# Kernel tuning notes

Hardware: AMD Instinct MI355X
Metric: run time of the kernel (lower is better)

Reference implementation:

```python
import jax, jax.numpy as jnp
import numpy as np

NUM_HEADS = 8
BLOCK_SIZE = 32   # tokens per block
WINDOW = 64       # window radius in blocks -> attends to blocks [i-64, i+64]


def setup_inputs() -> dict:
    key = jax.random.key(0)
    ks = jax.random.split(key, 5)
    B, N, C = 8, 8192, 512
    s = 0.02
    return {
        "x": jax.random.normal(ks[0], (B, N, C), dtype=jnp.float32),
        # torch Linear(dim, 3*dim): y = x @ W.T + b; we store W already transposed [in, out]
        "W_qkv": jax.random.normal(ks[1], (C, 3 * C), dtype=jnp.float32) * s,
        "b_qkv": jax.random.normal(ks[2], (3 * C,), dtype=jnp.float32) * s,
        "W_proj": jax.random.normal(ks[3], (C, C), dtype=jnp.float32) * s,
        "b_proj": jax.random.normal(ks[4], (C,), dtype=jnp.float32) * s,
    }


def reference(x, W_qkv, b_qkv, W_proj, b_proj):
    B, N, C = x.shape
    h = NUM_HEADS
    dh = C // h
    scale = jnp.asarray(dh, x.dtype) ** -0.5

    # qkv projection, then the module's head-interleaved split:
    # rearrange 'b n (h d) -> b h n d' with d = 3C/h, chunk(3) on last dim,
    # rearrange back 'b h n d -> b n (h d)'. Equivalent to:
    qkv = (x @ W_qkv + b_qkv).reshape(B, N, h, 3 * dh)
    q = qkv[..., :dh].reshape(B, N, C)
    k = qkv[..., dh:2 * dh].reshape(B, N, C)
    v = qkv[..., 2 * dh:].reshape(B, N, C)

    # dynamic blocking (N chosen divisible by BLOCK_SIZE -> no padding)
    nb = N // BLOCK_SIZE
    qb = q.reshape(B, nb, BLOCK_SIZE, C)
    kb = k.reshape(B, nb, BLOCK_SIZE, C)
    vb = v.reshape(B, nb, BLOCK_SIZE, C)

    # per-offset block attention: query block i, position s attends to
    # position s of every block j in [i-WINDOW, i+WINDOW]
    attn = jnp.einsum('bisc,bjsc->bisj', qb, kb) * scale  # [B, nb, s, nb]
    i_idx = jnp.arange(nb)[:, None]
    j_idx = jnp.arange(nb)[None, :]
    band = (j_idx >= i_idx - WINDOW) & (j_idx <= i_idx + WINDOW)  # [nb, nb]
    neg = jnp.finfo(attn.dtype).min
    attn = jnp.where(band[None, :, None, :], attn, neg)
    attn = jax.nn.softmax(attn, axis=-1)
    out = jnp.einsum('bisj,bjsc->bisc', attn, vb)  # [B, nb, s, C]
    out = out.reshape(B, N, C)

    # 'b n (h d) -> b n h d -> b n (h d)' is the identity
    return out @ W_proj + b_proj
```

## Files before the change

### kernel.cpp

```cpp
#include <hip/hip_runtime.h>
#include <hip/hip_bf16.h>
#include <stdint.h>

#define B_   8
#define N_   8192
#define C_   512
#define NB   256
#define WIN  64

typedef __attribute__((ext_vector_type(8))) short short8;
typedef __attribute__((ext_vector_type(4))) float f32x4;
typedef __hip_bfloat16 bf16;

__device__ __forceinline__ void gload_lds16(const void* g, void* l) {
  __builtin_amdgcn_global_load_lds((const __attribute__((address_space(1))) void*)g,
                                   (__attribute__((address_space(3))) void*)l, 16, 0, 0);
}

__device__ __forceinline__ f32x4 mfma16(short8 a, short8 b, f32x4 c) {
  return __builtin_amdgcn_mfma_f32_16x16x32_bf16(a, b, c, 0, 0, 0);
}


__global__ __launch_bounds__(256) void k_conv_x(const float4* __restrict__ x,
                                                ushort4* __restrict__ xb) {
  size_t idx = (size_t)blockIdx.x * 256 + threadIdx.x;
  float4 v = x[idx];
  union { ushort4 u; bf16 b[4]; } o;
  o.b[0] = __float2bfloat16(v.x); o.b[1] = __float2bfloat16(v.y);
  o.b[2] = __float2bfloat16(v.z); o.b[3] = __float2bfloat16(v.w);
  xb[idx] = o.u;
}

__global__ __launch_bounds__(256) void k_conv_w(const float* __restrict__ W,
                                                const float* __restrict__ bsrc,
                                                bf16* __restrict__ Wt,
                                                float* __restrict__ bperm,
                                                int ldw, int qkv) {
  __shared__ float tile[32][65];
  const int cc = blockIdx.x, k0 = blockIdx.y * 32;
  const int src0 = cc * 64;
  const int o0 = qkv ? ((cc % 3) * 512 + (cc / 3) * 64) : src0;
  const int tid = threadIdx.x;
#pragma unroll
  for (int q = 0; q < 8; ++q) {
    int li = q * 256 + tid;
    int r = li >> 6, c = li & 63;
    tile[r][c] = W[(size_t)(k0 + r) * ldw + src0 + c];
  }
  __syncthreads();
#pragma unroll
  for (int q = 0; q < 8; ++q) {
    int li = q * 256 + tid;
    int c2 = li >> 5, kk = li & 31;
    Wt[(size_t)(o0 + c2) * 512 + k0 + kk] = __float2bfloat16(tile[kk][c2]);
  }
  if (qkv && blockIdx.y == 0 && tid < 64) bperm[o0 + tid] = bsrc[src0 + tid];
}

#define WAITV(N) asm volatile("s_waitcnt vmcnt(" #N ")" ::: "memory")

template <int EPI>
__global__ __launch_bounds__(512, 2) void k_gemm(const bf16* __restrict__ A,
                                                 const bf16* __restrict__ Bt,
                                                 const float* __restrict__ bias,
                                                 bf16* __restrict__ qb,
                                                 bf16* __restrict__ kb,
                                                 bf16* __restrict__ vb,
                                                 float* __restrict__ outf,
                                                 int NTL) {
  extern __shared__ char gsm[];
  const int tid = threadIdx.x;
  const int lane = tid & 63, wid = tid >> 6;
  const int wr = wid >> 2, wcn = wid & 3;
  const int l15 = lane & 15, l4 = lane >> 4;
  const int sx = l15 & 7;

  const int T0 = blockIdx.x * NTL;

#define STAGE_A(E, H, K0, M0)                                                  \
  { _Pragma("unroll") for (int q = 0; q < 2; ++q) {                            \
      int li = q * 512 + tid;                                                  \
      int r = li >> 3, g = (li & 7) ^ (r & 7);                                 \
      gload_lds16(A + ((M0) + (H) * 128 + r) * 512 + (K0) + g * 8,             \
                  gsm + (E) * 65536 + (H) * 16384 + li * 16);                  \
    } }
#define STAGE_B(E, H, K0, N0)                                                  \
  { _Pragma("unroll") for (int q = 0; q < 2; ++q) {                            \
      int li = q * 512 + tid;                                                  \
      int r = li >> 3, g = (li & 7) ^ (r & 7);                                 \
      gload_lds16(Bt + (size_t)((N0) + (H) * 128 + r) * 512 + (K0) + g * 8,    \
                  gsm + (E) * 65536 + 32768 + (H) * 16384 + li * 16);          \
    } }

#define PHASE(FIH, FJH, LOADA, STAGE_STMT, WAIT_STMT)                          \
  {                                                                            \
    const char* Ab = gsm + d * 65536 + (FIH) * 16384;                          \
    const char* Bb = gsm + d * 65536 + 32768 + (FJH) * 16384;                  \
    if (LOADA) {                                                               \
      _Pragma("unroll") for (int f = 0; f < 4; ++f) {                          \
        int rA = f * 32 + wr * 16 + l15;                                       \
        af[f][0] = *(const short8*)(Ab + rA * 128 + ((l4 ^ sx) << 4));         \
        af[f][1] = *(const short8*)(Ab + rA * 128 + (((4 + l4) ^ sx) << 4));   \
      }                                                                        \
    }                                                                          \
    _Pragma("unroll") for (int f = 0; f < 2; ++f) {                            \
      int rB = f * 64 + wcn * 16 + l15;                                        \
      bfr[f][0] = *(const short8*)(Bb + rB * 128 + ((l4 ^ sx) << 4));          \
      bfr[f][1] = *(const short8*)(Bb + rB * 128 + (((4 + l4) ^ sx) << 4));    \
    }                                                                          \
    STAGE_STMT;                                                                \
    __builtin_amdgcn_sched_barrier(0);                                         \
    __builtin_amdgcn_s_barrier();                                              \
    __builtin_amdgcn_sched_barrier(0);                                         \
    __builtin_amdgcn_s_setprio(1);                                             \
    _Pragma("unroll") for (int f = 0; f < 4; ++f)                              \
      _Pragma("unroll") for (int g = 0; g < 2; ++g) {                          \
        acc[(FIH) * 4 + f][(FJH) * 2 + g] =                                    \
            mfma16(af[f][0], bfr[g][0], acc[(FIH) * 4 + f][(FJH) * 2 + g]);    \
        acc[(FIH) * 4 + f][(FJH) * 2 + g] =                                    \
            mfma16(af[f][1], bfr[g][1], acc[(FIH) * 4 + f][(FJH) * 2 + g]);    \
      }                                                                        \
    __builtin_amdgcn_s_setprio(0);                                             \
    __builtin_amdgcn_sched_barrier(0);                                         \
    WAIT_STMT;                                                                 \
    __builtin_amdgcn_s_barrier();                                              \
  }

  {
    const size_t m0p = (size_t)(T0 & 255) * 256;
    const int n0p = (T0 >> 8) * 256;
    STAGE_A(0, 0, 0, m0p); STAGE_B(0, 0, 0, n0p);
    STAGE_B(0, 1, 0, n0p); STAGE_A(0, 1, 0, m0p);
  }
  WAITV(4);
  __builtin_amdgcn_s_barrier();

  f32x4 acc[8][4];
  short8 af[4][2], bfr[2][2];

  for (int i = 0; i < NTL; ++i) {
    const int T = T0 + i;
    const size_t m0 = (size_t)(T & 255) * 256;
    const int n0 = (T >> 8) * 256;
    const size_t m0n = (size_t)((T + 1) & 255) * 256;
    const int n0n = ((T + 1) >> 8) * 256;

#pragma unroll
    for (int fi = 0; fi < 8; ++fi)
#pragma unroll
      for (int fj = 0; fj < 4; ++fj) acc[fi][fj] = (f32x4){0.f, 0.f, 0.f, 0.f};

    for (int t = 0; t < 8; ++t) {
      const int d = t & 1, e = d ^ 1;
      const bool more = (t < 7) || (i + 1 < NTL);
      const int kn = (t < 7) ? (t + 1) * 64 : 0;
      const size_t ma = (t < 7) ? m0 : m0n;
      const int nb = (t < 7) ? n0 : n0n;
      PHASE(0, 0, 1,
            { if (more) STAGE_A(e, 0, kn, ma); },
            { if (more) { WAITV(4); } else { WAITV(2); } });
      PHASE(0, 1, 0,
            { if (more) STAGE_B(e, 0, kn, nb); },
            { if (more) { WAITV(4); } else { WAITV(0); } });
      PHASE(1, 0, 1,
            { if (more) STAGE_B(e, 1, kn, nb); },
            { });
      PHASE(1, 1, 0,
            { if (more) STAGE_A(e, 1, kn, ma); },
            { if (more) { WAITV(4); } });
    }

    if (EPI == 0) {
#pragma unroll
      for (int fi = 0; fi < 8; ++fi)
#pragma unroll
        for (int fj = 0; fj < 4; ++fj) {
          int o = n0 + fj * 64 + wcn * 16 + l15;
          float bia = bias[o];
          int part = o >> 9;
          int c = o & 511;
          bf16* dst = part == 0 ? qb : (part == 1 ? kb : vb);
#pragma unroll
          for (int r = 0; r < 4; ++r) {
            size_t m = m0 + fi * 32 + wr * 16 + l4 * 4 + r;
            int bidx = (int)(m >> 13);
            int n = (int)(m & 8191);
            int blk = n >> 5, s = n & 31;
            size_t di = (((size_t)(bidx * 32 + s) * 256 + blk) << 9) | c;
            dst[di] = __float2bfloat16(acc[fi][fj][r] + bia);
          }
        }
    } else {
#pragma unroll
      for (int fi = 0; fi < 8; ++fi)
#pragma unroll
        for (int fj = 0; fj < 4; ++fj) {
          int o = n0 + fj * 64 + wcn * 16 + l15;
          float bia = bias[o];
#pragma unroll
          for (int r = 0; r < 4; ++r) {
            size_t m = m0 + fi * 32 + wr * 16 + l4 * 4 + r;
            outf[m * 512 + o] = acc[fi][fj][r] + bia;
          }
        }
    }
  }
#undef PHASE
#undef STAGE_A
#undef STAGE_B
}

__global__ __launch_bounds__(256) void k_transpose_v(const bf16* __restrict__ v,
                                                     bf16* __restrict__ vT) {
  __shared__ bf16 t[32][36];
  int bs = blockIdx.x, j0 = blockIdx.y * 32, c0 = blockIdx.z * 32;
  const bf16* src = v + (size_t)bs * NB * C_;
  bf16* dst = vT + (size_t)bs * C_ * NB;
  int r = threadIdx.x >> 3, c4 = (threadIdx.x & 7) * 4;
  *(ushort4*)&t[r][c4] = *(const ushort4*)(src + (size_t)(j0 + r) * C_ + c0 + c4);
  __syncthreads();
  union { ushort4 u; bf16 b[4]; } o;
  o.b[0] = t[c4 + 0][r]; o.b[1] = t[c4 + 1][r];
  o.b[2] = t[c4 + 2][r]; o.b[3] = t[c4 + 3][r];
  *(ushort4*)(dst + (size_t)(c0 + r) * NB + j0 + c4) = o.u;
}

#define KB_OFF   0
#define VB_OFF   65536
#define SS_OFF   98304
#define PS_OFF   102528
#define MR_OFF   105088
#define LR_OFF   105216
#define AL_OFF   105344
#define ATTN_LDS 105472

__global__ __launch_bounds__(512) void k_attn(const bf16* __restrict__ qg,
                                              const bf16* __restrict__ kg,
                                              const bf16* __restrict__ vTg,
                                              bf16* __restrict__ outb) {
  extern __shared__ char smc[];
  float* Ssf  = (float*)(smc + SS_OFF);
  bf16*  Psb  = (bf16*)(smc + PS_OFF);
  float* mrow = (float*)(smc + MR_OFF);
  float* lrow = (float*)(smc + LR_OFF);
  float* alph = (float*)(smc + AL_OFF);

  const int tid = threadIdx.x, lane = tid & 63, wid = tid >> 6;
  const int l15 = lane & 15, l4 = lane >> 4;
  const int gt = (blockIdx.x & 7) * 256 + (blockIdx.x >> 3);
  const int bs = gt >> 3;
  const int b = bs >> 5, s = bs & 31;
  const int i0 = (gt & 7) * 32;
  const int jlo = max(0, i0 - WIN);
  const int jhi = min(NB - 1, i0 + 31 + WIN);
  const int nch = (jhi - jlo + 1) >> 5;
  const bf16* Qb = qg + (size_t)bs * NB * C_;
  const bf16* Kb = kg + (size_t)bs * NB * C_;
  const bf16* Vb = vTg + (size_t)bs * C_ * NB;

  const int qhq = wid & 1, jhq = (wid >> 1) & 1;
  const int qh_pv = wid >> 2, cq = wid & 3;

  f32x4 O[8];
#pragma unroll
  for (int f = 0; f < 8; ++f) O[f] = (f32x4){0.f, 0.f, 0.f, 0.f};

  if (tid < 32) { mrow[tid] = -1e30f; lrow[tid] = 0.f; }

#pragma unroll
  for (int q = 0; q < 4; ++q) {
    int li = q * 512 + tid;
    int row = li >> 6, g = (li & 63) ^ (row & 15);
    gload_lds16(Kb + (size_t)(jlo + row) * C_ + g * 8, smc + KB_OFF + li * 16);
  }
  short8 qreg[16];
  if (wid < 4) {
    const bf16* qp = Qb + (size_t)(i0 + qhq * 16 + l15) * C_ + l4 * 8;
#pragma unroll
    for (int cc = 0; cc < 16; ++cc)
      qreg[cc] = *(const short8*)(qp + cc * 32);
  }

  for (int t = 0; t < nch; ++t) {
    const int j0 = jlo + t * 32;
    asm volatile("s_waitcnt lgkmcnt(0)" ::: "memory");
    __builtin_amdgcn_s_barrier();
    __builtin_amdgcn_sched_barrier(0);

#pragma unroll
    for (int q = 0; q < 4; ++q) {
      int li = q * 512 + tid;
      int c = li >> 2, g = (li & 3) ^ (c & 3);
      gload_lds16(Vb + (size_t)c * NB + j0 + g * 8, smc + VB_OFF + li * 16);
    }
    if (t + 1 < nch) {
      int jn = j0 + 32;
      char* kdst = smc + KB_OFF + ((t + 1) & 1) * 32768;
#pragma unroll
      for (int q = 0; q < 4; ++q) {
        int li = q * 512 + tid;
        int row = li >> 6, g = (li & 63) ^ (row & 15);
        gload_lds16(Kb + (size_t)(jn + row) * C_ + g * 8, kdst + li * 16);
      }
      asm volatile("s_waitcnt vmcnt(8)" ::: "memory");
    } else {
      asm volatile("s_waitcnt vmcnt(4)" ::: "memory");
    }
    __builtin_amdgcn_s_barrier();
    __builtin_amdgcn_sched_barrier(0);

    if (wid < 4) {
      const int brow = jhq * 16 + l15;
      const char* Kbase = smc + KB_OFF + (t & 1) * 32768 + brow * 1024;
      f32x4 a0 = (f32x4){0.f, 0.f, 0.f, 0.f}, a1 = a0;
      __builtin_amdgcn_s_setprio(1);
#pragma unroll
      for (int cc = 0; cc < 16; ++cc) {
        int sb = (cc * 4 + l4) ^ (brow & 15);
        short8 bv = *(const short8*)(Kbase + sb * 16);
        if (cc & 1) a1 = mfma16(qreg[cc], bv, a1);
        else        a0 = mfma16(qreg[cc], bv, a0);
      }
      __builtin_amdgcn_s_setprio(0);
      f32x4 su = a0 + a1;
      int jg = j0 + jhq * 16 + l15;
#pragma unroll
      for (int r = 0; r < 4; ++r) {
        int i_in = qhq * 16 + l4 * 4 + r;
        int i_abs = i0 + i_in;
        bool valid = (jg >= i_abs - WIN) && (jg <= i_abs + WIN);
        Ssf[i_in * 33 + jhq * 16 + l15] = valid ? su[r] * 0.125f : -1e30f;
      }
    }
    asm volatile("s_waitcnt lgkmcnt(0)" ::: "memory");
    __builtin_amdgcn_s_barrier();
    __builtin_amdgcn_sched_barrier(0);

    {
      int row = tid >> 4, u = tid & 15;
      float s0 = Ssf[row * 33 + u], s1 = Ssf[row * 33 + u + 16];
      float mc = fmaxf(s0, s1);
      mc = fmaxf(mc, __shfl_xor(mc, 1));
      mc = fmaxf(mc, __shfl_xor(mc, 2));
      mc = fmaxf(mc, __shfl_xor(mc, 4));
      mc = fmaxf(mc, __shfl_xor(mc, 8));
      float mo = mrow[row];
      float mn = fmaxf(mo, mc);
      float a = __expf(mo - mn);
      float p0 = __expf(s0 - mn), p1 = __expf(s1 - mn);
      float ps = p0 + p1;
      ps += __shfl_xor(ps, 1);
      ps += __shfl_xor(ps, 2);
      ps += __shfl_xor(ps, 4);
      ps += __shfl_xor(ps, 8);
      if (u == 0) {
        lrow[row] = lrow[row] * a + ps;
        mrow[row] = mn;
        alph[row] = a;
      }
      Psb[row * 40 + u] = __float2bfloat16(p0);
      Psb[row * 40 + u + 16] = __float2bfloat16(p1);
    }
    if (t + 1 < nch)
      asm volatile("s_waitcnt vmcnt(4) lgkmcnt(0)" ::: "memory");
    else
      asm volatile("s_waitcnt vmcnt(0) lgkmcnt(0)" ::: "memory");
    __builtin_amdgcn_s_barrier();
    __builtin_amdgcn_sched_barrier(0);

    {
      float ar[4];
#pragma unroll
      for (int r = 0; r < 4; ++r) ar[r] = alph[qh_pv * 16 + l4 * 4 + r];
      short8 pa = *(const short8*)(smc + PS_OFF + (qh_pv * 16 + l15) * 80 + l4 * 16);
      __builtin_amdgcn_s_setprio(1);
#pragma unroll
      for (int f = 0; f < 8; ++f) {
        int c = cq * 128 + f * 16 + l15;
        short8 vv = *(const short8*)(smc + VB_OFF + c * 64 + ((l4 ^ (c & 3)) << 4));
#pragma unroll
        for (int r = 0; r < 4; ++r) O[f][r] *= ar[r];
        O[f] = mfma16(pa, vv, O[f]);
      }
      __builtin_amdgcn_s_setprio(0);
    }
    __builtin_amdgcn_sched_barrier(0);
  }

  asm volatile("s_waitcnt lgkmcnt(0)" ::: "memory");
  __builtin_amdgcn_s_barrier();
  {
    float lr[4];
#pragma unroll
    for (int r = 0; r < 4; ++r) lr[r] = 1.f / lrow[qh_pv * 16 + l4 * 4 + r];
#pragma unroll
    for (int f = 0; f < 8; ++f) {
      int c = cq * 128 + f * 16 + l15;
#pragma unroll
      for (int r = 0; r < 4; ++r) {
        int il = qh_pv * 16 + l4 * 4 + r;
        int n = (i0 + il) * 32 + s;
        outb[((size_t)b * N_ + n) * C_ + c] = __float2bfloat16(O[f][r] * lr[r]);
      }
    }
  }
}

extern "C" void kernel_launch(void* const* d_in, const int* in_sizes, int n_in,
                              void* d_out, int out_size, void* d_ws, size_t ws_size,
                              hipStream_t stream) {
  const float* x = (const float*)d_in[0];
  const float* Wqkv = (const float*)d_in[1];
  const float* bqkv = (const float*)d_in[2];
  const float* Wproj = (const float*)d_in[3];
  const float* bproj = (const float*)d_in[4];

  char* ws = (char*)d_ws;
  const size_t SLOT = 67108864ull;
  bf16* slotA = (bf16*)ws;
  bf16* slotB = (bf16*)(ws + SLOT);
  bf16* Wqkv_t = (bf16*)(ws + 2 * SLOT);
  bf16* Wproj_t = (bf16*)(ws + 2 * SLOT + 1572864);
  float* bias_perm = (float*)(ws + 2 * SLOT + 1572864 + 524288);
  bf16* qbuf = (bf16*)d_out;
  bf16* kbuf = qbuf + 33554432ull;

  static int attr_done = 0;
  if (!attr_done) {
    hipFuncSetAttribute((const void*)k_gemm<0>,
                        hipFuncAttributeMaxDynamicSharedMemorySize, 131072);
    hipFuncSetAttribute((const void*)k_gemm<1>,
                        hipFuncAttributeMaxDynamicSharedMemorySize, 131072);
    hipFuncSetAttribute((const void*)k_attn,
                        hipFuncAttributeMaxDynamicSharedMemorySize, ATTN_LDS);
    attr_done = 1;
  }

  k_conv_x<<<32768, 256, 0, stream>>>((const float4*)x, (ushort4*)slotA);
  k_conv_w<<<dim3(24, 16), 256, 0, stream>>>(Wqkv, bqkv, Wqkv_t, bias_perm, 1536, 1);
  k_conv_w<<<dim3(8, 16), 256, 0, stream>>>(Wproj, nullptr, Wproj_t, nullptr, 512, 0);

  k_gemm<0><<<256, 512, 131072, stream>>>(slotA, Wqkv_t, bias_perm,
                                          qbuf, kbuf, slotB, nullptr, 6);
  k_transpose_v<<<dim3(256, 8, 16), 256, 0, stream>>>(slotB, slotA);
  k_attn<<<2048, 512, ATTN_LDS, stream>>>(qbuf, kbuf, slotA, slotB);
  k_gemm<1><<<256, 512, 131072, stream>>>(slotB, Wproj_t, bproj,
                                          nullptr, nullptr, nullptr, (float*)d_out, 2);
}
```

Before: 339.1 us.

## Load GEMM B operand directly from global into registers, skipping LDS staging

The GEMM kernel no longer stages the weight (B) tiles through LDS. Each wave reads its B fragments straight from global memory into registers every k-step, while only the A tile stays double-buffered in LDS. This halves the LDS footprint to 64KB and cuts barrier phases from four to two per k-step. The cost is that B fragments are loaded redundantly by each wave row, with global latency exposed directly before the MFMAs, and many more registers are held for B fragments.

```diff
diff --git a/kernel.cpp b/kernel.cpp
--- a/kernel.cpp
+++ b/kernel.cpp
@@ -83,43 +83,33 @@
       int li = q * 512 + tid;                                                  \
       int r = li >> 3, g = (li & 7) ^ (r & 7);                                 \
       gload_lds16(A + ((M0) + (H) * 128 + r) * 512 + (K0) + g * 8,             \
-                  gsm + (E) * 65536 + (H) * 16384 + li * 16);                  \
+                  gsm + (E) * 32768 + (H) * 16384 + li * 16);                  \
     } }
-#define STAGE_B(E, H, K0, N0)                                                  \
-  { _Pragma("unroll") for (int q = 0; q < 2; ++q) {                            \
-      int li = q * 512 + tid;                                                  \
-      int r = li >> 3, g = (li & 7) ^ (r & 7);                                 \
-      gload_lds16(Bt + (size_t)((N0) + (H) * 128 + r) * 512 + (K0) + g * 8,    \
-                  gsm + (E) * 65536 + 32768 + (H) * 16384 + li * 16);          \
-    } }
-
-#define PHASE(FIH, FJH, LOADA, STAGE_STMT, WAIT_STMT)                          \
+
+#define PHASE2(H, STAGE_STMT, WAIT_STMT)                                       \
   {                                                                            \
-    const char* Ab = gsm + d * 65536 + (FIH) * 16384;                          \
-    const char* Bb = gsm + d * 65536 + 32768 + (FJH) * 16384;                  \
-    if (LOADA) {                                                               \
-      _Pragma("unroll") for (int f = 0; f < 4; ++f) {                          \
-        int rA = f * 32 + wr * 16 + l15;                                       \
-        af[f][0] = *(const short8*)(Ab + rA * 128 + ((l4 ^ sx) << 4));         \
-        af[f][1] = *(const short8*)(Ab + rA * 128 + (((4 + l4) ^ sx) << 4));   \
-      }                                                                        \
+    const char* Ab = gsm + d * 32768;                                          \
+    _Pragma("unroll") for (int f = 0; f < 4; ++f) {                            \
+      int rA = ((H) * 4 + f) * 32 + wr * 16 + l15;                             \
+      af[f][0] = *(const short8*)(Ab + rA * 128 + ((l4 ^ sx) << 4));           \
+      af[f][1] = *(const short8*)(Ab + rA * 128 + (((4 + l4) ^ sx) << 4));     \
     }                                                                          \
-    _Pragma("unroll") for (int f = 0; f < 2; ++f) {                            \
-      int rB = f * 64 + wcn * 16 + l15;                                        \
-      bfr[f][0] = *(const short8*)(Bb + rB * 128 + ((l4 ^ sx) << 4));          \
-      bfr[f][1] = *(const short8*)(Bb + rB * 128 + (((4 + l4) ^ sx) << 4));    \
+    _Pragma("unroll") for (int f = 0; f < 4; ++f) {                            \
+      int rb = f * 64 + wcn * 16 + l15;                                        \
+      const bf16* bp = Bt + (size_t)(n0 + rb) * 512 + t * 64 + l4 * 8;         \
+      bfr[f][0] = *(const short8*)bp;                                          \
+      bfr[f][1] = *(const short8*)(bp + 32);                                   \
     }                                                                          \
+    __builtin_amdgcn_sched_barrier(0);                                         \
     STAGE_STMT;                                                                \
     __builtin_amdgcn_sched_barrier(0);                                         \
     __builtin_amdgcn_s_barrier();                                              \
     __builtin_amdgcn_sched_barrier(0);                                         \
     __builtin_amdgcn_s_setprio(1);                                             \
     _Pragma("unroll") for (int f = 0; f < 4; ++f)                              \
-      _Pragma("unroll") for (int g = 0; g < 2; ++g) {                          \
-        acc[(FIH) * 4 + f][(FJH) * 2 + g] =                                    \
-            mfma16(af[f][0], bfr[g][0], acc[(FIH) * 4 + f][(FJH) * 2 + g]);    \
-        acc[(FIH) * 4 + f][(FJH) * 2 + g] =                                    \
-            mfma16(af[f][1], bfr[g][1], acc[(FIH) * 4 + f][(FJH) * 2 + g]);    \
+      _Pragma("unroll") for (int g = 0; g < 4; ++g) {                          \
+        acc[(H) * 4 + f][g] = mfma16(af[f][0], bfr[g][0], acc[(H) * 4 + f][g]);\
+        acc[(H) * 4 + f][g] = mfma16(af[f][1], bfr[g][1], acc[(H) * 4 + f][g]);\
       }                                                                        \
     __builtin_amdgcn_s_setprio(0);                                             \
     __builtin_amdgcn_sched_barrier(0);                                         \
@@ -129,22 +119,20 @@
 
   {
     const size_t m0p = (size_t)(T0 & 255) * 256;
-    const int n0p = (T0 >> 8) * 256;
-    STAGE_A(0, 0, 0, m0p); STAGE_B(0, 0, 0, n0p);
-    STAGE_B(0, 1, 0, n0p); STAGE_A(0, 1, 0, m0p);
-  }
-  WAITV(4);
+    STAGE_A(0, 0, 0, m0p);
+    STAGE_A(0, 1, 0, m0p);
+  }
+  WAITV(2);
   __builtin_amdgcn_s_barrier();
 
   f32x4 acc[8][4];
-  short8 af[4][2], bfr[2][2];
+  short8 af[4][2], bfr[4][2];
 
   for (int i = 0; i < NTL; ++i) {
     const int T = T0 + i;
     const size_t m0 = (size_t)(T & 255) * 256;
     const int n0 = (T >> 8) * 256;
     const size_t m0n = (size_t)((T + 1) & 255) * 256;
-    const int n0n = ((T + 1) >> 8) * 256;
 
 #pragma unroll
     for (int fi = 0; fi < 8; ++fi)
@@ -156,19 +144,12 @@
       const bool more = (t < 7) || (i + 1 < NTL);
       const int kn = (t < 7) ? (t + 1) * 64 : 0;
       const size_t ma = (t < 7) ? m0 : m0n;
-      const int nb = (t < 7) ? n0 : n0n;
-      PHASE(0, 0, 1,
-            { if (more) STAGE_A(e, 0, kn, ma); },
-            { if (more) { WAITV(4); } else { WAITV(2); } });
-      PHASE(0, 1, 0,
-            { if (more) STAGE_B(e, 0, kn, nb); },
-            { if (more) { WAITV(4); } else { WAITV(0); } });
-      PHASE(1, 0, 1,
-            { if (more) STAGE_B(e, 1, kn, nb); },
-            { });
-      PHASE(1, 1, 0,
-            { if (more) STAGE_A(e, 1, kn, ma); },
-            { if (more) { WAITV(4); } });
+      PHASE2(0,
+             { if (more) STAGE_A(e, 0, kn, ma); },
+             { if (more) { WAITV(2); } else { WAITV(0); } });
+      PHASE2(1,
+             { if (more) STAGE_A(e, 1, kn, ma); },
+             { if (more) { WAITV(2); } });
     }
 
     if (EPI == 0) {
@@ -206,9 +187,8 @@
         }
     }
   }
-#undef PHASE
+#undef PHASE2
 #undef STAGE_A
-#undef STAGE_B
 }
 
 __global__ __launch_bounds__(256) void k_transpose_v(const bf16* __restrict__ v,
@@ -429,9 +409,9 @@
   static int attr_done = 0;
   if (!attr_done) {
     hipFuncSetAttribute((const void*)k_gemm<0>,
-                        hipFuncAttributeMaxDynamicSharedMemorySize, 131072);
+                        hipFuncAttributeMaxDynamicSharedMemorySize, 65536);
     hipFuncSetAttribute((const void*)k_gemm<1>,
-                        hipFuncAttributeMaxDynamicSharedMemorySize, 131072);
+                        hipFuncAttributeMaxDynamicSharedMemorySize, 65536);
     hipFuncSetAttribute((const void*)k_attn,
                         hipFuncAttributeMaxDynamicSharedMemorySize, ATTN_LDS);
     attr_done = 1;
@@ -441,10 +421,10 @@
   k_conv_w<<<dim3(24, 16), 256, 0, stream>>>(Wqkv, bqkv, Wqkv_t, bias_perm, 1536, 1);
   k_conv_w<<<dim3(8, 16), 256, 0, stream>>>(Wproj, nullptr, Wproj_t, nullptr, 512, 0);
 
-  k_gemm<0><<<256, 512, 131072, stream>>>(slotA, Wqkv_t, bias_perm,
-                                          qbuf, kbuf, slotB, nullptr, 6);
+  k_gemm<0><<<256, 512, 65536, stream>>>(slotA, Wqkv_t, bias_perm,
+                                         qbuf, kbuf, slotB, nullptr, 6);
   k_transpose_v<<<dim3(256, 8, 16), 256, 0, stream>>>(slotB, slotA);
   k_attn<<<2048, 512, ATTN_LDS, stream>>>(qbuf, kbuf, slotA, slotB);
-  k_gemm<1><<<256, 512, 131072, stream>>>(slotB, Wproj_t, bproj,
-                                          nullptr, nullptr, nullptr, (float*)d_out, 2);
-}
+  k_gemm<1><<<256, 512, 65536, stream>>>(slotB, Wproj_t, bproj,
+                                         nullptr, nullptr, nullptr, (float*)d_out, 2);
+}
```

Result: slower. 440.5 us (+29.9%).
